# Kernel optimization log

Hardware: AMD Instinct MI355X
Metric: run time of the kernel (lower is better)

Reference implementation:

```python
import jax, jax.numpy as jnp
import numpy as np

EPS = 0.001  # numerical_stabilizer


def setup_inputs() -> dict:
    key = jax.random.key(0)
    ks = jax.random.split(key, 8)
    B, L, D, H, M = 4, 4096, 1024, 16, 64
    scale = 0.02
    return {
        "query": jax.random.normal(ks[0], (B, L, D), jnp.float32),
        "key": jax.random.normal(ks[1], (B, L, D), jnp.float32),
        "value": jax.random.normal(ks[2], (B, L, D), jnp.float32),
        "Wq": jax.random.normal(ks[3], (D, H, M), jnp.float32) * scale,
        "bq": jnp.zeros((H, M), jnp.float32),
        "Wk": jax.random.normal(ks[4], (D, H, M), jnp.float32) * scale,
        "bk": jnp.zeros((H, M), jnp.float32),
        "Wv": jax.random.normal(ks[5], (D, H, M), jnp.float32) * scale,
        "bv": jnp.zeros((H, M), jnp.float32),
        "Wo": jax.random.normal(ks[6], (H, M, D), jnp.float32) * scale,
        "bo": jnp.zeros((D,), jnp.float32),
        "step": 0,
    }


def reference(query, key, value, Wq, bq, Wk, bk, Wv, bv, Wo, bo, step):
    # QKV projections: [B,L,D] x [D,H,M] -> [B,L,H,M]
    q = jnp.einsum('bld,dhm->blhm', query, Wq) + bq
    k = jnp.einsum('bld,dhm->blhm', key, Wk) + bk
    v = jnp.einsum('bld,dhm->blhm', value, Wv) + bv
    # ReLU feature map with stabilizer
    q = jax.nn.relu(q) + EPS
    k = jax.nn.relu(k) + EPS
    # Linear (kernelized) attention: KV outer-product state [B,H,M,M]
    kvs = jnp.einsum('blhm,blhd->bhmd', k, v)
    a_v = jnp.einsum('blhm,bhmd->blhd', q, kvs)
    # Normalizer: sum of keys over sequence
    ks_sum = jnp.sum(k, axis=1)                       # [B,H,M]
    norm = jnp.einsum('blhm,bhm->blh', q, ks_sum)     # [B,L,H]
    a_v = a_v / norm[..., None]
    # Output projection over (head, head_dim) -> hidden
    out = jnp.einsum('blhm,hmd->bld', a_v, Wo) + bo
    return out
```

## Files before the change

### kernel.cpp

```cpp
#include <hip/hip_runtime.h>
#include <stdint.h>


typedef __bf16 bf16;
typedef __bf16 bf16x4 __attribute__((ext_vector_type(4)));
typedef __bf16 bf16x8 __attribute__((ext_vector_type(8)));
typedef float f32x4 __attribute__((ext_vector_type(4)));

#define MFMA_(a, b, c) __builtin_amdgcn_mfma_f32_16x16x32_bf16((a), (b), (c), 0, 0, 0)

static constexpr int BB   = 4;
static constexpr int LSEQ = 4096;
static constexpr int DIM  = 1024;
static constexpr int HH   = 16;
static constexpr float EPSF = 0.001f;

__device__ __forceinline__ void gload16(bf16* lds, const bf16* g) {
  __builtin_amdgcn_global_load_lds(
      (const __attribute__((address_space(1))) void*)g,
      (__attribute__((address_space(3))) void*)lds, 16, 0, 0);
}

__device__ __forceinline__ void stage128(bf16* lds, const bf16* src, size_t ld,
                                         int wid, int lane) {
#pragma unroll
  for (int j = 0; j < 4; ++j) {
    const int chunk = wid * 4 + j;
    const int e = chunk * 512 + lane * 8;
    gload16(lds + chunk * 512, src + (size_t)(e >> 6) * ld + (e & 63));
  }
}

__global__ void k_cvt(const float* __restrict__ q, const float* __restrict__ k,
                      const float* __restrict__ v, bf16* __restrict__ xb) {
  const int nchunk = 3 << 21;
  const int stride = gridDim.x * blockDim.x;
  for (int c = blockIdx.x * blockDim.x + threadIdx.x; c < nchunk; c += stride) {
    const int t = c >> 21;
    const size_t off = (size_t)(c & ((1 << 21) - 1)) * 8;
    const float* src = (t == 0) ? q : (t == 1) ? k : v;
    const f32x4* sp = reinterpret_cast<const f32x4*>(src + off);
    const f32x4 a = __builtin_nontemporal_load(sp);
    const f32x4 b = __builtin_nontemporal_load(sp + 1);
    bf16x8 o;
    o[0] = (bf16)a[0]; o[1] = (bf16)a[1]; o[2] = (bf16)a[2]; o[3] = (bf16)a[3];
    o[4] = (bf16)b[0]; o[5] = (bf16)b[1]; o[6] = (bf16)b[2]; o[7] = (bf16)b[3];
    *reinterpret_cast<bf16x8*>(xb + (size_t)t * 16777216u + off) = o;
  }
}

__global__ void k_prep_w4(const float* __restrict__ W0, const float* __restrict__ W1,
                          const float* __restrict__ W2, const float* __restrict__ W3,
                          bf16* __restrict__ T0, bf16* __restrict__ T1,
                          bf16* __restrict__ T2, bf16* __restrict__ T3) {
  const float* W; bf16* T;
  switch (blockIdx.z) {
    case 0:  W = W0; T = T0; break;
    case 1:  W = W1; T = T1; break;
    case 2:  W = W2; T = T2; break;
    default: W = W3; T = T3; break;
  }
  __shared__ float t[32][33];
  const int tx = threadIdx.x & 31, ty = threadIdx.x >> 5;
  const int r0 = blockIdx.x * 32, c0 = blockIdx.y * 32;
#pragma unroll
  for (int j = 0; j < 32; j += 8)
    t[ty + j][tx] = W[(size_t)(r0 + ty + j) * DIM + c0 + tx];
  __syncthreads();
#pragma unroll
  for (int j = 0; j < 32; j += 8)
    T[(size_t)(c0 + ty + j) * DIM + r0 + tx] = (bf16)t[tx][ty + j];
}

__global__ void k_init_vt(bf16* __restrict__ vt) {
  const int c = blockIdx.x * 256 + threadIdx.x;
  const int l8 = c & 511;
  const int r  = (c >> 9) & 15;
  const int bh = c >> 13;
  const bf16 val = (r == 0) ? (bf16)1.0f : (bf16)0.0f;
  bf16x8 o;
#pragma unroll
  for (int j = 0; j < 8; ++j) o[j] = val;
  *reinterpret_cast<bf16x8*>(vt + ((size_t)bh * 80 + 64 + r) * LSEQ + l8 * 8) = o;
}

template <int MODE>
__global__ void k_proj(const bf16* __restrict__ X, const bf16* __restrict__ WT,
                       const float* __restrict__ bias, bf16* __restrict__ out) {
  __shared__ bf16 As[128 * 64];
  __shared__ bf16 Bs[128 * 64];
  const int tid = threadIdx.x, lane = tid & 63, wid = tid >> 6;
  const int wr = wid >> 1, wc = wid & 1;
  const int lr = lane & 15, lk = lane >> 4;
  const int n0 = blockIdx.x * 128, c0 = blockIdx.y * 128;
  f32x4 acc[4][4] = {};

  for (int ks = 0; ks < 16; ++ks) {
    const int k0 = ks * 64;
    __syncthreads();
    stage128(As, X + (size_t)n0 * DIM + k0, DIM, wid, lane);
    stage128(Bs, WT + (size_t)c0 * DIM + k0, DIM, wid, lane);
    __syncthreads();
#pragma unroll
    for (int kk = 0; kk < 2; ++kk) {
      bf16x8 af[4], bfr[4];
#pragma unroll
      for (int rb = 0; rb < 4; ++rb)
        af[rb] = *reinterpret_cast<const bf16x8*>(&As[(wr * 64 + rb * 16 + lr) * 64 + kk * 32 + lk * 8]);
#pragma unroll
      for (int cb = 0; cb < 4; ++cb)
        bfr[cb] = *reinterpret_cast<const bf16x8*>(&Bs[(wc * 64 + cb * 16 + lr) * 64 + kk * 32 + lk * 8]);
#pragma unroll
      for (int rb = 0; rb < 4; ++rb)
#pragma unroll
        for (int cb = 0; cb < 4; ++cb)
          acc[rb][cb] = MFMA_(af[rb], bfr[cb], acc[rb][cb]);
    }
  }

  float bvv[4];
#pragma unroll
  for (int cb = 0; cb < 4; ++cb) bvv[cb] = bias[c0 + wc * 64 + cb * 16 + lr];
  const int bidx = n0 >> 12;
  const int l0 = n0 & (LSEQ - 1);
#pragma unroll
  for (int rb = 0; rb < 4; ++rb) {
#pragma unroll
    for (int cb = 0; cb < 4; ++cb) {
      const int c = c0 + wc * 64 + cb * 16 + lr;
      if (MODE == 0) {
#pragma unroll
        for (int r = 0; r < 4; ++r) {
          float x = acc[rb][cb][r] + bvv[cb];
          x = fmaxf(x, 0.f) + EPSF;
          const int row = n0 + wr * 64 + rb * 16 + lk * 4 + r;
          out[(size_t)row * DIM + c] = (bf16)x;
        }
      } else {
        const int l = l0 + wr * 64 + rb * 16 + lk * 4;
        bf16x4 o;
#pragma unroll
        for (int r = 0; r < 4; ++r) {
          float x = acc[rb][cb][r] + bvv[cb];
          if (MODE == 1) x = fmaxf(x, 0.f) + EPSF;
          o[r] = (bf16)x;
        }
        size_t rowbase;
        if (MODE == 1) rowbase = (size_t)bidx * 1024 + c;
        else           rowbase = ((size_t)(bidx * HH + (c >> 6)) * 80 + (c & 63));
        *reinterpret_cast<bf16x4*>(out + rowbase * LSEQ + l) = o;
      }
    }
  }
}

__global__ __launch_bounds__(256, 2) void k_kvs(const bf16* __restrict__ kt,
                                                const bf16* __restrict__ vt,
                                                float* __restrict__ kvs) {
  const int tid = threadIdx.x, lane = tid & 63, wid = tid >> 6;
  const int lr = lane & 15, lk = lane >> 4;
  const int bh = blockIdx.y;
  const int lbase = blockIdx.x * 512;
  __shared__ bf16 As[64][64];
  __shared__ bf16 Bs[80][64];
  f32x4 acc[5] = {};
  const bf16* ktb = kt + (size_t)bh * 64 * LSEQ;
  const bf16* vtb = vt + (size_t)bh * 80 * LSEQ;

  for (int ks = 0; ks < 8; ++ks) {
    const int l0 = lbase + ks * 64;
    __syncthreads();
#pragma unroll
    for (int i = 0; i < 2; ++i) {
      const int e = i * 2048 + tid * 8;
      const int row = e >> 6, col = e & 63;
      *reinterpret_cast<bf16x8*>(&As[row][col]) =
          *reinterpret_cast<const bf16x8*>(ktb + (size_t)row * LSEQ + l0 + col);
    }
#pragma unroll
    for (int i = 0; i < 2; ++i) {
      const int e = i * 2048 + tid * 8;
      const int row = e >> 6, col = e & 63;
      *reinterpret_cast<bf16x8*>(&Bs[row][col]) =
          *reinterpret_cast<const bf16x8*>(vtb + (size_t)row * LSEQ + l0 + col);
    }
    if (tid < 128) {
      const int e = 4096 + tid * 8;
      const int row = e >> 6, col = e & 63;
      *reinterpret_cast<bf16x8*>(&Bs[row][col]) =
          *reinterpret_cast<const bf16x8*>(vtb + (size_t)row * LSEQ + l0 + col);
    }
    __syncthreads();
#pragma unroll
    for (int kk = 0; kk < 2; ++kk) {
      const bf16x8 af = *reinterpret_cast<const bf16x8*>(&As[wid * 16 + lr][kk * 32 + lk * 8]);
#pragma unroll
      for (int cb = 0; cb < 5; ++cb) {
        const bf16x8 bfr = *reinterpret_cast<const bf16x8*>(&Bs[cb * 16 + lr][kk * 32 + lk * 8]);
        acc[cb] = MFMA_(af, bfr, acc[cb]);
      }
    }
  }
  float* kb = kvs + (size_t)bh * 64 * 80;
#pragma unroll
  for (int cb = 0; cb < 5; ++cb) {
    const int dcol = cb * 16 + lr;
#pragma unroll
    for (int r = 0; r < 4; ++r) {
      const int m = wid * 16 + lk * 4 + r;
      atomicAdd(kb + m * 80 + dcol, acc[cb][r]);
    }
  }
}

__global__ void k_kvs_t(const float* __restrict__ kvs, bf16* __restrict__ bav) {
  const int bh = blockIdx.x;
  const float* src = kvs + (size_t)bh * 5120;
  bf16* dst = bav + (size_t)bh * 5120;
  for (int i = threadIdx.x; i < 5120; i += 256) {
    const int dp = i >> 6, mm = i & 63;
    dst[i] = (bf16)src[mm * 80 + dp];
  }
}

__global__ __launch_bounds__(256, 2) void k_av(const bf16* __restrict__ q,
                                               const bf16* __restrict__ bav,
                                               bf16* __restrict__ avn) {
  const int tid = threadIdx.x, lane = tid & 63, wid = tid >> 6;
  const int lr = lane & 15, lk = lane >> 4;
  const int bh = blockIdx.y, b = bh >> 4, h = bh & 15;
  const int l0 = blockIdx.x * 128;
  __shared__ bf16 As[128][64];
  __shared__ bf16 Bs[80][64];
  __shared__ float nrm[128];

  const bf16* qb = q + ((size_t)b * LSEQ + l0) * DIM + h * 64;
#pragma unroll
  for (int i = 0; i < 4; ++i) {
    const int e = i * 2048 + tid * 8;
    const int row = e >> 6, col = e & 63;
    *reinterpret_cast<bf16x8*>(&As[row][col]) =
        *reinterpret_cast<const bf16x8*>(qb + (size_t)row * DIM + col);
  }
  const bf16* bb = bav + (size_t)bh * 5120;
#pragma unroll
  for (int i = 0; i < 2; ++i) {
    const int e = i * 2048 + tid * 8;
    const int row = e >> 6, col = e & 63;
    *reinterpret_cast<bf16x8*>(&Bs[row][col]) =
        *reinterpret_cast<const bf16x8*>(bb + row * 64 + col);
  }
  if (tid < 128) {
    const int e = 4096 + tid * 8;
    const int row = e >> 6, col = e & 63;
    *reinterpret_cast<bf16x8*>(&Bs[row][col]) =
        *reinterpret_cast<const bf16x8*>(bb + row * 64 + col);
  }
  __syncthreads();

  f32x4 acc[2][5] = {};
#pragma unroll
  for (int kk = 0; kk < 2; ++kk) {
    bf16x8 af[2];
    af[0] = *reinterpret_cast<const bf16x8*>(&As[wid * 32 + lr][kk * 32 + lk * 8]);
    af[1] = *reinterpret_cast<const bf16x8*>(&As[wid * 32 + 16 + lr][kk * 32 + lk * 8]);
#pragma unroll
    for (int cb = 0; cb < 5; ++cb) {
      const bf16x8 bfr = *reinterpret_cast<const bf16x8*>(&Bs[cb * 16 + lr][kk * 32 + lk * 8]);
      acc[0][cb] = MFMA_(af[0], bfr, acc[0][cb]);
      acc[1][cb] = MFMA_(af[1], bfr, acc[1][cb]);
    }
  }
  if (lr == 0) {
#pragma unroll
    for (int rb = 0; rb < 2; ++rb)
#pragma unroll
      for (int r = 0; r < 4; ++r)
        nrm[wid * 32 + rb * 16 + lk * 4 + r] = acc[rb][4][r];
  }
  __syncthreads();
  bf16* ob = avn + ((size_t)b * LSEQ + l0) * DIM + h * 64;
#pragma unroll
  for (int rb = 0; rb < 2; ++rb) {
#pragma unroll
    for (int cb = 0; cb < 4; ++cb) {
#pragma unroll
      for (int r = 0; r < 4; ++r) {
        const int row = wid * 32 + rb * 16 + lk * 4 + r;
        const float x = acc[rb][cb][r] / nrm[row];
        ob[(size_t)row * DIM + cb * 16 + lr] = (bf16)x;
      }
    }
  }
}

__global__ void k_out(const bf16* __restrict__ A, const bf16* __restrict__ WoT,
                      const float* __restrict__ bo, float* __restrict__ out) {
  __shared__ bf16 As[128 * 64];
  __shared__ bf16 Bs[128 * 64];
  const int tid = threadIdx.x, lane = tid & 63, wid = tid >> 6;
  const int wr = wid >> 1, wc = wid & 1;
  const int lr = lane & 15, lk = lane >> 4;
  const int n0 = blockIdx.x * 128, c0 = blockIdx.y * 128;
  f32x4 acc[4][4] = {};

  for (int ks = 0; ks < 16; ++ks) {
    const int k0 = ks * 64;
    __syncthreads();
    stage128(As, A + (size_t)n0 * DIM + k0, DIM, wid, lane);
    stage128(Bs, WoT + (size_t)c0 * DIM + k0, DIM, wid, lane);
    __syncthreads();
#pragma unroll
    for (int kk = 0; kk < 2; ++kk) {
      bf16x8 af[4], bfr[4];
#pragma unroll
      for (int rb = 0; rb < 4; ++rb)
        af[rb] = *reinterpret_cast<const bf16x8*>(&As[(wr * 64 + rb * 16 + lr) * 64 + kk * 32 + lk * 8]);
#pragma unroll
      for (int cb = 0; cb < 4; ++cb)
        bfr[cb] = *reinterpret_cast<const bf16x8*>(&Bs[(wc * 64 + cb * 16 + lr) * 64 + kk * 32 + lk * 8]);
#pragma unroll
      for (int rb = 0; rb < 4; ++rb)
#pragma unroll
        for (int cb = 0; cb < 4; ++cb)
          acc[rb][cb] = MFMA_(af[rb], bfr[cb], acc[rb][cb]);
    }
  }
  float bvv[4];
#pragma unroll
  for (int cb = 0; cb < 4; ++cb) bvv[cb] = bo[c0 + wc * 64 + cb * 16 + lr];
#pragma unroll
  for (int rb = 0; rb < 4; ++rb)
#pragma unroll
    for (int cb = 0; cb < 4; ++cb)
#pragma unroll
      for (int r = 0; r < 4; ++r) {
        const int row = n0 + wr * 64 + rb * 16 + lk * 4 + r;
        const int c = c0 + wc * 64 + cb * 16 + lr;
        out[(size_t)row * DIM + c] = acc[rb][cb][r] + bvv[cb];
      }
}

extern "C" void kernel_launch(void* const* d_in, const int* in_sizes, int n_in,
                              void* d_out, int out_size, void* d_ws, size_t ws_size,
                              hipStream_t stream) {
  const float* query = (const float*)d_in[0];
  const float* key   = (const float*)d_in[1];
  const float* value = (const float*)d_in[2];
  const float* Wq    = (const float*)d_in[3];
  const float* bq    = (const float*)d_in[4];
  const float* Wk    = (const float*)d_in[5];
  const float* bk    = (const float*)d_in[6];
  const float* Wv    = (const float*)d_in[7];
  const float* bvp   = (const float*)d_in[8];
  const float* Wo    = (const float*)d_in[9];
  const float* bo    = (const float*)d_in[10];
  float* out = (float*)d_out;
  char* ws = (char*)d_ws;

  const size_t off_wqt = 0;
  const size_t off_wkt = off_wqt + (2u << 20);
  const size_t off_wvt = off_wkt + (2u << 20);
  const size_t off_wot = off_wvt + (2u << 20);
  const size_t off_xb  = off_wot + (2u << 20);
  const size_t off_vt  = off_xb  + 100663296ull;
  const size_t off_kvs = off_vt  + 41943040ull;
  const size_t off_bav = off_kvs + 1310720ull;
  const size_t total   = off_bav + 655360ull;
  if (ws_size < total) return;

  bf16*  WQT = (bf16*)(ws + off_wqt);
  bf16*  WKT = (bf16*)(ws + off_wkt);
  bf16*  WVT = (bf16*)(ws + off_wvt);
  bf16*  WOT = (bf16*)(ws + off_wot);
  bf16*  XB  = (bf16*)(ws + off_xb);
  bf16*  XBq = XB;
  bf16*  XBk = XB + 16777216u;
  bf16*  XBv = XB + 33554432u;
  bf16*  VT  = (bf16*)(ws + off_vt);
  float* KVS = (float*)(ws + off_kvs);
  bf16*  BAV = (bf16*)(ws + off_bav);
  bf16*  KT  = XBv;
  bf16*  Qb  = XBk;
  bf16*  AV  = XBq;

  k_cvt<<<2048, 256, 0, stream>>>(query, key, value, XB);
  k_prep_w4<<<dim3(32, 32, 4), 256, 0, stream>>>(Wq, Wk, Wv, Wo, WQT, WKT, WVT, WOT);
  k_init_vt<<<2048, 256, 0, stream>>>(VT);
  (void)hipMemsetAsync(KVS, 0, 1310720ull, stream);

  k_proj<2><<<dim3(128, 8), 256, 0, stream>>>(XBv, WVT, bvp, VT);
  k_proj<1><<<dim3(128, 8), 256, 0, stream>>>(XBk, WKT, bk, KT);
  k_proj<0><<<dim3(128, 8), 256, 0, stream>>>(XBq, WQT, bq, Qb);

  k_kvs<<<dim3(8, 64), 256, 0, stream>>>(KT, VT, KVS);
  k_kvs_t<<<64, 256, 0, stream>>>(KVS, BAV);

  k_av<<<dim3(32, 64), 256, 0, stream>>>(Qb, BAV, AV);

  k_out<<<dim3(128, 8), 256, 0, stream>>>(AV, WOT, bo, out);
}
```

Before: 280.2 us.

## Replace projection GEMMs with 256x256 double-buffered pipelined MFMA kernel

Replaces the 128x128 single-buffered projection and output GEMMs with one templated 256x256-tile kernel using 512 threads, double-buffered LDS, and an interleaved schedule. Global-to-LDS loads are issued in half-tile chunks between MFMA phases with explicit vmcnt waits, barriers and setprio. An XOR swizzle on LDS columns is meant to reduce bank conflicts. The aim is to hide load latency and raise MFMA utilisation. The larger tiles cut the grid to 256 blocks, which under-fills the CUs, and the hand-tuned waitcnt sequencing is fragile.

```diff
diff --git a/kernel.cpp b/kernel.cpp
--- a/kernel.cpp
+++ b/kernel.cpp
@@ -19,16 +19,6 @@
   __builtin_amdgcn_global_load_lds(
       (const __attribute__((address_space(1))) void*)g,
       (__attribute__((address_space(3))) void*)lds, 16, 0, 0);
-}
-
-__device__ __forceinline__ void stage128(bf16* lds, const bf16* src, size_t ld,
-                                         int wid, int lane) {
-#pragma unroll
-  for (int j = 0; j < 4; ++j) {
-    const int chunk = wid * 4 + j;
-    const int e = chunk * 512 + lane * 8;
-    gload16(lds + chunk * 512, src + (size_t)(e >> 6) * ld + (e & 63));
-  }
 }
 
 __global__ void k_cvt(const float* __restrict__ q, const float* __restrict__ k,
@@ -84,64 +74,127 @@
   *reinterpret_cast<bf16x8*>(vt + ((size_t)bh * 80 + 64 + r) * LSEQ + l8 * 8) = o;
 }
 
+__device__ __forceinline__ void stage_half(bf16 (&As)[2][16384], bf16 (&Bs)[2][16384],
+                                           const bf16* Ab, const bf16* Bb,
+                                           int h, int w, int srow, int scol) {
+  const int t = h >> 2, reg = h & 3, buf = t & 1;
+  bf16* lds = (reg < 2) ? &As[buf][(reg & 1) * 8192] : &Bs[buf][(reg & 1) * 8192];
+  const bf16* g = (reg < 2) ? Ab : Bb;
+  const int rbase = (reg & 1) * 128;
+#pragma unroll
+  for (int rr = 0; rr < 2; ++rr) {
+    const int row = rbase + (rr * 8 + w) * 8 + srow;
+    gload16(lds + (rr * 8 + w) * 512, g + (size_t)row * DIM + t * 64 + scol);
+  }
+}
+
+#define LDA(d, g, f)                                                                              \
+  a[d][0] = *reinterpret_cast<const bf16x8*>(&As[g][(wm * 128 + (f) * 16 + lr) * 64 + colb]);     \
+  a[d][1] = *reinterpret_cast<const bf16x8*>(&As[g][(wm * 128 + (f) * 16 + lr) * 64 + 32 + colb]);
+#define LDB(d, g, c)                                                                              \
+  b[d][0] = *reinterpret_cast<const bf16x8*>(&Bs[g][(wn * 64 + (c) * 16 + lr) * 64 + colb]);      \
+  b[d][1] = *reinterpret_cast<const bf16x8*>(&Bs[g][(wn * 64 + (c) * 16 + lr) * 64 + 32 + colb]);
+#define MM(fi, ci, fo, co)                                                                        \
+  acc[fo][co] = MFMA_(a[fi][0], b[ci][0], acc[fo][co]);                                           \
+  acc[fo][co] = MFMA_(a[fi][1], b[ci][1], acc[fo][co]);
+
+#define PHASE(g, q, pidx)                                                                         \
+  {                                                                                               \
+    if ((q) == 0) { LDA(0, g, 0) LDA(1, g, 1) LDA(2, g, 2) LDA(3, g, 3)                           \
+                    LDB(0, g, 0) LDB(1, g, 1) }                                                   \
+    else if ((q) == 1) { LDB(0, g, 2) LDB(1, g, 3) }                                              \
+    else if ((q) == 2) { LDA(0, g, 4) LDA(1, g, 5) LDA(2, g, 6) LDA(3, g, 7) }                    \
+    else { LDB(0, g, 0) LDB(1, g, 1) }                                                            \
+    const int hh = 8 * i + 5 + (pidx);                                                            \
+    if (hh < 64) stage_half(As, Bs, Ab, Bb, hh, w, srow, scol);                                   \
+    if ((pidx) == 3 || (pidx) == 7) {                                                             \
+      if (i < 7) { asm volatile("s_waitcnt vmcnt(2)" ::: "memory"); }                             \
+      else       { asm volatile("s_waitcnt vmcnt(0)" ::: "memory"); }                             \
+    }                                                                                             \
+    __builtin_amdgcn_sched_barrier(0);                                                            \
+    __builtin_amdgcn_s_barrier();                                                                 \
+    __builtin_amdgcn_sched_barrier(0);                                                            \
+    __builtin_amdgcn_s_setprio(1);                                                                \
+    if ((q) == 0) { MM(0, 0, 0, 0) MM(1, 0, 1, 0) MM(2, 0, 2, 0) MM(3, 0, 3, 0)                   \
+                    MM(0, 1, 0, 1) MM(1, 1, 1, 1) MM(2, 1, 2, 1) MM(3, 1, 3, 1) }                 \
+    else if ((q) == 1) { MM(0, 0, 0, 2) MM(1, 0, 1, 2) MM(2, 0, 2, 2) MM(3, 0, 3, 2)              \
+                         MM(0, 1, 0, 3) MM(1, 1, 1, 3) MM(2, 1, 2, 3) MM(3, 1, 3, 3) }            \
+    else if ((q) == 2) { MM(0, 0, 4, 2) MM(1, 0, 5, 2) MM(2, 0, 6, 2) MM(3, 0, 7, 2)              \
+                         MM(0, 1, 4, 3) MM(1, 1, 5, 3) MM(2, 1, 6, 3) MM(3, 1, 7, 3) }            \
+    else { MM(0, 0, 4, 0) MM(1, 0, 5, 0) MM(2, 0, 6, 0) MM(3, 0, 7, 0)                            \
+           MM(0, 1, 4, 1) MM(1, 1, 5, 1) MM(2, 1, 6, 1) MM(3, 1, 7, 1) }                          \
+    __builtin_amdgcn_s_setprio(0);                                                                \
+    __builtin_amdgcn_sched_barrier(0);                                                            \
+    __builtin_amdgcn_s_barrier();                                                                 \
+    __builtin_amdgcn_sched_barrier(0);                                                            \
+  }
+
 template <int MODE>
-__global__ void k_proj(const bf16* __restrict__ X, const bf16* __restrict__ WT,
-                       const float* __restrict__ bias, bf16* __restrict__ out) {
-  __shared__ bf16 As[128 * 64];
-  __shared__ bf16 Bs[128 * 64];
-  const int tid = threadIdx.x, lane = tid & 63, wid = tid >> 6;
-  const int wr = wid >> 1, wc = wid & 1;
-  const int lr = lane & 15, lk = lane >> 4;
-  const int n0 = blockIdx.x * 128, c0 = blockIdx.y * 128;
-  f32x4 acc[4][4] = {};
-
-  for (int ks = 0; ks < 16; ++ks) {
-    const int k0 = ks * 64;
-    __syncthreads();
-    stage128(As, X + (size_t)n0 * DIM + k0, DIM, wid, lane);
-    stage128(Bs, WT + (size_t)c0 * DIM + k0, DIM, wid, lane);
-    __syncthreads();
-#pragma unroll
-    for (int kk = 0; kk < 2; ++kk) {
-      bf16x8 af[4], bfr[4];
-#pragma unroll
-      for (int rb = 0; rb < 4; ++rb)
-        af[rb] = *reinterpret_cast<const bf16x8*>(&As[(wr * 64 + rb * 16 + lr) * 64 + kk * 32 + lk * 8]);
-#pragma unroll
-      for (int cb = 0; cb < 4; ++cb)
-        bfr[cb] = *reinterpret_cast<const bf16x8*>(&Bs[(wc * 64 + cb * 16 + lr) * 64 + kk * 32 + lk * 8]);
-#pragma unroll
-      for (int rb = 0; rb < 4; ++rb)
-#pragma unroll
-        for (int cb = 0; cb < 4; ++cb)
-          acc[rb][cb] = MFMA_(af[rb], bfr[cb], acc[rb][cb]);
-    }
+__global__ __launch_bounds__(512, 2) void k_gemm256(const bf16* __restrict__ X,
+                                                    const bf16* __restrict__ WT,
+                                                    const float* __restrict__ bias,
+                                                    void* __restrict__ outp) {
+  __shared__ __align__(16) bf16 As[2][16384];
+  __shared__ __align__(16) bf16 Bs[2][16384];
+  const int tid = threadIdx.x;
+  const int lane = tid & 63, w = tid >> 6;
+  const int wm = w >> 2, wn = w & 3;
+  const int lr = lane & 15, lk = (lane >> 4) & 3;
+  const int n0 = blockIdx.x * 256, c0 = blockIdx.y * 256;
+  const int colb = (lk * 8) ^ ((lane & 4) ? 16 : 0);
+  const int srow = lane >> 3;
+  const int scol = ((lane & 7) * 8) ^ ((lane & 32) >> 1);
+  const bf16* Ab = X + (size_t)n0 * DIM;
+  const bf16* Bb = WT + (size_t)c0 * DIM;
+
+  f32x4 acc[8][4] = {};
+  bf16x8 a[4][2], b[2][2];
+
+#pragma unroll
+  for (int h = 0; h < 5; ++h) stage_half(As, Bs, Ab, Bb, h, w, srow, scol);
+  asm volatile("s_waitcnt vmcnt(2)" ::: "memory");
+  __builtin_amdgcn_sched_barrier(0);
+  __builtin_amdgcn_s_barrier();
+  __builtin_amdgcn_sched_barrier(0);
+
+  for (int i = 0; i < 8; ++i) {
+    PHASE(0, 0, 0) PHASE(0, 1, 1) PHASE(0, 2, 2) PHASE(0, 3, 3)
+    PHASE(1, 0, 4) PHASE(1, 1, 5) PHASE(1, 2, 6) PHASE(1, 3, 7)
   }
 
   float bvv[4];
 #pragma unroll
-  for (int cb = 0; cb < 4; ++cb) bvv[cb] = bias[c0 + wc * 64 + cb * 16 + lr];
+  for (int cb = 0; cb < 4; ++cb) bvv[cb] = bias[c0 + wn * 64 + cb * 16 + lr];
   const int bidx = n0 >> 12;
   const int l0 = n0 & (LSEQ - 1);
 #pragma unroll
-  for (int rb = 0; rb < 4; ++rb) {
+  for (int f = 0; f < 8; ++f) {
 #pragma unroll
     for (int cb = 0; cb < 4; ++cb) {
-      const int c = c0 + wc * 64 + cb * 16 + lr;
+      const int c = c0 + wn * 64 + cb * 16 + lr;
       if (MODE == 0) {
+        bf16* out = (bf16*)outp;
 #pragma unroll
         for (int r = 0; r < 4; ++r) {
-          float x = acc[rb][cb][r] + bvv[cb];
+          float x = acc[f][cb][r] + bvv[cb];
           x = fmaxf(x, 0.f) + EPSF;
-          const int row = n0 + wr * 64 + rb * 16 + lk * 4 + r;
+          const int row = n0 + wm * 128 + f * 16 + lk * 4 + r;
           out[(size_t)row * DIM + c] = (bf16)x;
         }
+      } else if (MODE == 3) {
+        float* out = (float*)outp;
+#pragma unroll
+        for (int r = 0; r < 4; ++r) {
+          const int row = n0 + wm * 128 + f * 16 + lk * 4 + r;
+          out[(size_t)row * DIM + c] = acc[f][cb][r] + bvv[cb];
+        }
       } else {
-        const int l = l0 + wr * 64 + rb * 16 + lk * 4;
+        bf16* out = (bf16*)outp;
+        const int l = l0 + wm * 128 + f * 16 + lk * 4;
         bf16x4 o;
 #pragma unroll
         for (int r = 0; r < 4; ++r) {
-          float x = acc[rb][cb][r] + bvv[cb];
+          float x = acc[f][cb][r] + bvv[cb];
           if (MODE == 1) x = fmaxf(x, 0.f) + EPSF;
           o[r] = (bf16)x;
         }
@@ -153,6 +206,10 @@
     }
   }
 }
+#undef PHASE
+#undef MM
+#undef LDB
+#undef LDA
 
 __global__ __launch_bounds__(256, 2) void k_kvs(const bf16* __restrict__ kt,
                                                 const bf16* __restrict__ vt,
@@ -292,53 +349,6 @@
       }
     }
   }
-}
-
-__global__ void k_out(const bf16* __restrict__ A, const bf16* __restrict__ WoT,
-                      const float* __restrict__ bo, float* __restrict__ out) {
-  __shared__ bf16 As[128 * 64];
-  __shared__ bf16 Bs[128 * 64];
-  const int tid = threadIdx.x, lane = tid & 63, wid = tid >> 6;
-  const int wr = wid >> 1, wc = wid & 1;
-  const int lr = lane & 15, lk = lane >> 4;
-  const int n0 = blockIdx.x * 128, c0 = blockIdx.y * 128;
-  f32x4 acc[4][4] = {};
-
-  for (int ks = 0; ks < 16; ++ks) {
-    const int k0 = ks * 64;
-    __syncthreads();
-    stage128(As, A + (size_t)n0 * DIM + k0, DIM, wid, lane);
-    stage128(Bs, WoT + (size_t)c0 * DIM + k0, DIM, wid, lane);
-    __syncthreads();
-#pragma unroll
-    for (int kk = 0; kk < 2; ++kk) {
-      bf16x8 af[4], bfr[4];
-#pragma unroll
-      for (int rb = 0; rb < 4; ++rb)
-        af[rb] = *reinterpret_cast<const bf16x8*>(&As[(wr * 64 + rb * 16 + lr) * 64 + kk * 32 + lk * 8]);
-#pragma unroll
-      for (int cb = 0; cb < 4; ++cb)
-        bfr[cb] = *reinterpret_cast<const bf16x8*>(&Bs[(wc * 64 + cb * 16 + lr) * 64 + kk * 32 + lk * 8]);
-#pragma unroll
-      for (int rb = 0; rb < 4; ++rb)
-#pragma unroll
-        for (int cb = 0; cb < 4; ++cb)
-          acc[rb][cb] = MFMA_(af[rb], bfr[cb], acc[rb][cb]);
-    }
-  }
-  float bvv[4];
-#pragma unroll
-  for (int cb = 0; cb < 4; ++cb) bvv[cb] = bo[c0 + wc * 64 + cb * 16 + lr];
-#pragma unroll
-  for (int rb = 0; rb < 4; ++rb)
-#pragma unroll
-    for (int cb = 0; cb < 4; ++cb)
-#pragma unroll
-      for (int r = 0; r < 4; ++r) {
-        const int row = n0 + wr * 64 + rb * 16 + lk * 4 + r;
-        const int c = c0 + wc * 64 + cb * 16 + lr;
-        out[(size_t)row * DIM + c] = acc[rb][cb][r] + bvv[cb];
-      }
 }
 
 extern "C" void kernel_launch(void* const* d_in, const int* in_sizes, int n_in,
@@ -389,14 +399,14 @@
   k_init_vt<<<2048, 256, 0, stream>>>(VT);
   (void)hipMemsetAsync(KVS, 0, 1310720ull, stream);
 
-  k_proj<2><<<dim3(128, 8), 256, 0, stream>>>(XBv, WVT, bvp, VT);
-  k_proj<1><<<dim3(128, 8), 256, 0, stream>>>(XBk, WKT, bk, KT);
-  k_proj<0><<<dim3(128, 8), 256, 0, stream>>>(XBq, WQT, bq, Qb);
+  k_gemm256<2><<<dim3(64, 4), 512, 0, stream>>>(XBv, WVT, bvp, VT);
+  k_gemm256<1><<<dim3(64, 4), 512, 0, stream>>>(XBk, WKT, bk, KT);
+  k_gemm256<0><<<dim3(64, 4), 512, 0, stream>>>(XBq, WQT, bq, Qb);
 
   k_kvs<<<dim3(8, 64), 256, 0, stream>>>(KT, VT, KVS);
   k_kvs_t<<<64, 256, 0, stream>>>(KVS, BAV);
 
   k_av<<<dim3(32, 64), 256, 0, stream>>>(Qb, BAV, AV);
 
-  k_out<<<dim3(128, 8), 256, 0, stream>>>(AV, WOT, bo, out);
-}
+  k_gemm256<3><<<dim3(64, 4), 512, 0, stream>>>(AV, WOT, bo, out);
+}
```

Result: no change. 282.4 us (+0.8%).
